# Kernel tuning notes

Measured on AMD Instinct MI355X. Metric: run time of the kernel, lower is better.

## Reference

```python
import jax, jax.numpy as jnp
import numpy as np

NEG_SLOPE = 0.01  # torch nn.LeakyReLU default


def setup_inputs() -> dict:
    key = jax.random.key(0)
    k1, k2, k3, k4, k5 = jax.random.split(key, 5)
    B, C, N, O = 32, 512, 1024, 512
    x = jax.random.normal(k1, (B, C, N), dtype=jnp.float32)
    wq = jax.random.normal(k2, (C,), dtype=jnp.float32) * (1.0 / np.sqrt(C))
    wk = jax.random.normal(k3, (C,), dtype=jnp.float32) * (1.0 / np.sqrt(C))
    wm = jax.random.normal(k4, (O, C), dtype=jnp.float32) * (1.0 / np.sqrt(C))
    bm = jax.random.normal(k5, (O,), dtype=jnp.float32) * 0.01
    return {"x": x, "wq": wq, "wk": wk, "wm": wm, "bm": bm}


def reference(x, wq, wk, wm, bm):
    # x: [B, C, N]
    q = jnp.einsum('c,bcn->bn', wq, x)            # [B, N] (Conv1d C->1, k=1, no bias)
    k = jnp.einsum('c,bcn->bn', wk, x)            # [B, N]
    scores = q[:, None, :] + k[:, :, None]        # [B, N, N] additive broadcast
    scores = jnp.where(scores > 0, scores, NEG_SLOPE * scores)  # LeakyReLU
    att = jax.nn.softmax(scores, axis=-1)         # softmax over last dim
    agg = jnp.einsum('bcn,bmn->bcm', x, att)      # weighted aggregation [B, C, N]
    out = jnp.einsum('oc,bcm->bom', wm, agg) + bm[None, :, None]  # Conv1d k=1
    return jax.nn.relu(out)
```

## Files before the change

### kernel.cpp

```cpp
#include <hip/hip_runtime.h>


constexpr int B = 32, C = 512, N = 1024, O = 512;
constexpr float L2E = 1.4426950408889634f;

typedef _Float16 half8 __attribute__((ext_vector_type(8)));
typedef _Float16 half4v __attribute__((ext_vector_type(4)));
typedef _Float16 half2v __attribute__((ext_vector_type(2)));
typedef float f32x4 __attribute__((ext_vector_type(4)));

#if __has_builtin(__builtin_amdgcn_exp2f)
#define EXP2(x) __builtin_amdgcn_exp2f(x)
#else
#define EXP2(x) exp2f(x)
#endif

__device__ __forceinline__ half8 cvt8(float4 a, float4 b) {
  half8 h;
  h[0] = (_Float16)a.x; h[1] = (_Float16)a.y; h[2] = (_Float16)a.z; h[3] = (_Float16)a.w;
  h[4] = (_Float16)b.x; h[5] = (_Float16)b.y; h[6] = (_Float16)b.z; h[7] = (_Float16)b.w;
  return h;
}

__device__ __forceinline__ unsigned fenc(float x) {
  unsigned u = __float_as_uint(x);
  return (u & 0x80000000u) ? ~u : (u ^ 0x80000000u);
}
__device__ __forceinline__ float fdec(unsigned e) {
  unsigned u = (e & 0x80000000u) ? (e ^ 0x80000000u) : ~e;
  return __uint_as_float(u);
}

__global__ __launch_bounds__(256) void wmh_kernel(const float* __restrict__ wm,
                                                  _Float16* __restrict__ wmh) {
  int i = (blockIdx.x * 256 + threadIdx.x) * 8;
  float4 a = *(const float4*)(wm + i);
  float4 b = *(const float4*)(wm + i + 4);
  *(half8*)(wmh + i) = cvt8(a, b);
}

__global__ __launch_bounds__(256) void gemm_y_kernel(const float* __restrict__ x,
    const _Float16* __restrict__ wmh, const float* __restrict__ wq,
    const float* __restrict__ wk, float* __restrict__ q, float* __restrict__ k,
    unsigned* __restrict__ qmax_u, _Float16* __restrict__ Yt) {
  __shared__ half2v Xs[16 * 130];
  __shared__ float mred[4];
  int b  = blockIdx.y;
  int n0 = blockIdx.x * 128;
  int o0 = blockIdx.z * 128;
  int t = threadIdx.x;
  int w = t >> 6, l = t & 63;
  int nw = w >> 1, ow = w & 1;
  int lm = l & 15, q8 = (l >> 4) * 8, q4 = (l >> 4) * 4;

  int cp = t >> 4, ng = t & 15;
  bool doqk = (blockIdx.z == 0);
  float aq[8] = {}, ak[8] = {};

  const _Float16* wb[4];
#pragma unroll
  for (int j = 0; j < 4; ++j)
    wb[j] = wmh + (size_t)(o0 + ow * 64 + j * 16 + lm) * C + q8;

  f32x4 acc[4][4] = {};
  for (int c0 = 0; c0 < C; c0 += 32) {
    const float* xr = x + ((size_t)b * C + c0 + 2 * cp) * N + n0 + ng * 8;
    float4 a0 = *(const float4*)(xr);
    float4 a1 = *(const float4*)(xr + 4);
    float4 b0 = *(const float4*)(xr + N);
    float4 b1 = *(const float4*)(xr + N + 4);
    half8 bf[4];
#pragma unroll
    for (int j = 0; j < 4; ++j) bf[j] = *(const half8*)(wb[j] + c0);

    if (doqk) {
      float2 wq2 = *(const float2*)&wq[c0 + 2 * cp];
      float2 wk2 = *(const float2*)&wk[c0 + 2 * cp];
      aq[0] = fmaf(wq2.x, a0.x, fmaf(wq2.y, b0.x, aq[0]));
      aq[1] = fmaf(wq2.x, a0.y, fmaf(wq2.y, b0.y, aq[1]));
      aq[2] = fmaf(wq2.x, a0.z, fmaf(wq2.y, b0.z, aq[2]));
      aq[3] = fmaf(wq2.x, a0.w, fmaf(wq2.y, b0.w, aq[3]));
      aq[4] = fmaf(wq2.x, a1.x, fmaf(wq2.y, b1.x, aq[4]));
      aq[5] = fmaf(wq2.x, a1.y, fmaf(wq2.y, b1.y, aq[5]));
      aq[6] = fmaf(wq2.x, a1.z, fmaf(wq2.y, b1.z, aq[6]));
      aq[7] = fmaf(wq2.x, a1.w, fmaf(wq2.y, b1.w, aq[7]));
      ak[0] = fmaf(wk2.x, a0.x, fmaf(wk2.y, b0.x, ak[0]));
      ak[1] = fmaf(wk2.x, a0.y, fmaf(wk2.y, b0.y, ak[1]));
      ak[2] = fmaf(wk2.x, a0.z, fmaf(wk2.y, b0.z, ak[2]));
      ak[3] = fmaf(wk2.x, a0.w, fmaf(wk2.y, b0.w, ak[3]));
      ak[4] = fmaf(wk2.x, a1.x, fmaf(wk2.y, b1.x, ak[4]));
      ak[5] = fmaf(wk2.x, a1.y, fmaf(wk2.y, b1.y, ak[5]));
      ak[6] = fmaf(wk2.x, a1.z, fmaf(wk2.y, b1.z, ak[6]));
      ak[7] = fmaf(wk2.x, a1.w, fmaf(wk2.y, b1.w, ak[7]));
    }

    __syncthreads();
    {
      half2v* xp = &Xs[cp * 130 + ng * 8];
      xp[0] = half2v{(_Float16)a0.x, (_Float16)b0.x};
      xp[1] = half2v{(_Float16)a0.y, (_Float16)b0.y};
      xp[2] = half2v{(_Float16)a0.z, (_Float16)b0.z};
      xp[3] = half2v{(_Float16)a0.w, (_Float16)b0.w};
      xp[4] = half2v{(_Float16)a1.x, (_Float16)b1.x};
      xp[5] = half2v{(_Float16)a1.y, (_Float16)b1.y};
      xp[6] = half2v{(_Float16)a1.z, (_Float16)b1.z};
      xp[7] = half2v{(_Float16)a1.w, (_Float16)b1.w};
    }
    __syncthreads();

    half8 af[4];
#pragma unroll
    for (int i = 0; i < 4; ++i) {
      int nrow = nw * 64 + i * 16 + lm;
#pragma unroll
      for (int jp = 0; jp < 4; ++jp) {
        half2v p = Xs[(q4 + jp) * 130 + nrow];
        af[i][2 * jp]     = p[0];
        af[i][2 * jp + 1] = p[1];
      }
    }
#pragma unroll
    for (int i = 0; i < 4; ++i)
#pragma unroll
      for (int j = 0; j < 4; ++j)
        acc[i][j] = __builtin_amdgcn_mfma_f32_16x16x32_f16(af[i], bf[j], acc[i][j], 0, 0, 0);
  }

#pragma unroll
  for (int i = 0; i < 4; ++i) {
    int n_b = n0 + nw * 64 + i * 16 + (l >> 4) * 4;
#pragma unroll
    for (int j = 0; j < 4; ++j) {
      int o_c = o0 + ow * 64 + j * 16 + lm;
      half4v h;
      h[0] = (_Float16)acc[i][j][0];
      h[1] = (_Float16)acc[i][j][1];
      h[2] = (_Float16)acc[i][j][2];
      h[3] = (_Float16)acc[i][j][3];
      *(half4v*)&Yt[((size_t)b * O + o_c) * N + n_b] = h;
    }
  }

  if (doqk) {
    float* red = (float*)Xs;
    float qv_final = -1e30f;
    __syncthreads();
#pragma unroll
    for (int j = 0; j < 8; ++j) red[cp * 130 + ng * 8 + j] = aq[j];
    __syncthreads();
    if (t < 128) {
      float s = 0.f;
#pragma unroll
      for (int p = 0; p < 16; ++p) s += red[p * 130 + t];
      qv_final = L2E * s;
      q[b * N + n0 + t] = qv_final;
    }
    __syncthreads();
#pragma unroll
    for (int j = 0; j < 8; ++j) red[cp * 130 + ng * 8 + j] = ak[j];
    __syncthreads();
    if (t < 128) {
      float s = 0.f;
#pragma unroll
      for (int p = 0; p < 16; ++p) s += red[p * 130 + t];
      k[b * N + n0 + t] = L2E * s;
    }
    float m = qv_final;
#pragma unroll
    for (int off = 32; off > 0; off >>= 1) m = fmaxf(m, __shfl_down(m, off, 64));
    if ((t & 63) == 0) mred[t >> 6] = m;
    __syncthreads();
    if (t == 0) {
      float bmax = fmaxf(fmaxf(mred[0], mred[1]), fmaxf(mred[2], mred[3]));
      atomicMax(&qmax_u[b], fenc(bmax));
    }
  }
}

__global__ __launch_bounds__(256) void gemm_out_kernel(const _Float16* __restrict__ Yt,
    const float* __restrict__ q, const float* __restrict__ k,
    const unsigned* __restrict__ qmax_u, const float* __restrict__ bm,
    float* __restrict__ out) {
  __shared__ __align__(16) float qs[N];
  __shared__ __align__(16) _Float16 Ys[128 * 40];
  __shared__ float izs[128];
  int b  = blockIdx.y;
  int o0 = blockIdx.x * 128;
  int m0 = blockIdx.z * 128;
  int t = threadIdx.x;
  int w = t >> 6, l = t & 63;
  int lm = l & 15, g = l >> 4, q8 = g * 8;

  *(float4*)&qs[t * 4] = *(const float4*)&q[b * N + t * 4];

  float qmv = fdec(qmax_u[b]);
  float k2[2], k3[2];
#pragma unroll
  for (int i = 0; i < 2; ++i) {
    float km = k[b * N + m0 + w * 32 + i * 16 + lm];
    float s0 = qmv + km;
    float M  = fmaxf(s0, 0.01f * s0);
    k2[i] = km - M;
    k3[i] = fmaf(0.01f, km, -M);
  }
  half8 ones;
#pragma unroll
  for (int jj = 0; jj < 8; ++jj) ones[jj] = (_Float16)1.0f;
  f32x4 acc_z[2] = {};
  int yr = t >> 1, yp = t & 1;
  const _Float16* ysrc = Yt + ((size_t)b * O + o0 + yr) * N + yp * 16;
  __syncthreads();

  f32x4 acc[2][8] = {};
  for (int n0k = 0; n0k < N; n0k += 32) {
    half8 y0 = *(const half8*)(ysrc + n0k);
    half8 y1 = *(const half8*)(ysrc + n0k + 8);
    float4 qa = *(const float4*)&qs[n0k + q8];
    float4 qb = *(const float4*)&qs[n0k + q8 + 4];
    float qv[8] = {qa.x, qa.y, qa.z, qa.w, qb.x, qb.y, qb.z, qb.w};
    half8 af[2];
#pragma unroll
    for (int i = 0; i < 2; ++i) {
#pragma unroll
      for (int jj = 0; jj < 8; ++jj) {
        float arg = fmaxf(qv[jj] + k2[i], fmaf(0.01f, qv[jj], k3[i]));
        af[i][jj] = (_Float16)EXP2(arg);
      }
      acc_z[i] = __builtin_amdgcn_mfma_f32_16x16x32_f16(af[i], ones, acc_z[i], 0, 0, 0);
    }
    __syncthreads();
    *(half8*)&Ys[yr * 40 + yp * 16]     = y0;
    *(half8*)&Ys[yr * 40 + yp * 16 + 8] = y1;
    __syncthreads();

    half8 bf[8];
#pragma unroll
    for (int j = 0; j < 8; ++j)
      bf[j] = *(const half8*)&Ys[(j * 16 + lm) * 40 + q8];
#pragma unroll
    for (int i = 0; i < 2; ++i)
#pragma unroll
      for (int j = 0; j < 8; ++j)
        acc[i][j] = __builtin_amdgcn_mfma_f32_16x16x32_f16(af[i], bf[j], acc[i][j], 0, 0, 0);
  }

  if (lm == 0) {
#pragma unroll
    for (int i = 0; i < 2; ++i) {
#pragma unroll
      for (int r = 0; r < 4; ++r)
        izs[w * 32 + i * 16 + g * 4 + r] = 1.0f / acc_z[i][r];
    }
  }
  __syncthreads();

  float iz4v[2][4];
#pragma unroll
  for (int i = 0; i < 2; ++i) {
    float4 iz4 = *(const float4*)&izs[w * 32 + i * 16 + g * 4];
    iz4v[i][0] = iz4.x; iz4v[i][1] = iz4.y; iz4v[i][2] = iz4.z; iz4v[i][3] = iz4.w;
  }
#pragma unroll
  for (int j = 0; j < 8; ++j) {
    int o_c = o0 + j * 16 + lm;
    float bias = bm[o_c];
#pragma unroll
    for (int i = 0; i < 2; ++i) {
      int m_b = m0 + w * 32 + i * 16 + g * 4;
      float4 r;
      r.x = fmaxf(fmaf(acc[i][j][0], iz4v[i][0], bias), 0.f);
      r.y = fmaxf(fmaf(acc[i][j][1], iz4v[i][1], bias), 0.f);
      r.z = fmaxf(fmaf(acc[i][j][2], iz4v[i][2], bias), 0.f);
      r.w = fmaxf(fmaf(acc[i][j][3], iz4v[i][3], bias), 0.f);
      *(float4*)&out[((size_t)b * O + o_c) * N + m_b] = r;
    }
  }
}

extern "C" void kernel_launch(void* const* d_in, const int* in_sizes, int n_in,
                              void* d_out, int out_size, void* d_ws, size_t ws_size,
                              hipStream_t stream) {
  const float* x  = (const float*)d_in[0];
  const float* wq = (const float*)d_in[1];
  const float* wk = (const float*)d_in[2];
  const float* wm = (const float*)d_in[3];
  const float* bm = (const float*)d_in[4];
  float* out = (float*)d_out;

  float* q    = (float*)d_ws;
  float* k    = q + B * N;
  unsigned* qmax_u = (unsigned*)(k + B * N);
  _Float16* wmh = (_Float16*)(qmax_u + 64);
  _Float16* Yt  = wmh + (size_t)O * C;

  hipMemsetAsync(qmax_u, 0, 64 * sizeof(unsigned), stream);
  wmh_kernel<<<dim3(O * C / (256 * 8)), 256, 0, stream>>>(wm, wmh);
  gemm_y_kernel<<<dim3(N / 128, B, O / 128), 256, 0, stream>>>(x, wmh, wq, wk, q, k, qmax_u, Yt);
  gemm_out_kernel<<<dim3(O / 128, B, N / 128), 256, 0, stream>>>(Yt, q, k, qmax_u, bm, out);
}
```

Measured before the change: 216.3 us.

## Widen output-GEMM tile to 256 o-columns with 512 threads, drop memset

The output GEMM kernel now covers 256 output channels per block with 8 waves, each wave owning 16 m-rows instead of 32. Each wave therefore computes the exp-softmax weights once and reuses them across 16 column tiles, which cuts the redundant exp work per output across o-blocks in half. The qmax reset memset is folded into the weight-conversion kernel, saving one launch. In exchange the block uses more LDS and more accumulator registers per thread, which may lower occupancy.

Result: faster. 210.4 us (-2.7%).

```diff
diff --git a/kernel.cpp b/kernel.cpp
--- a/kernel.cpp
+++ b/kernel.cpp
@@ -32,11 +32,13 @@
 }
 
 __global__ __launch_bounds__(256) void wmh_kernel(const float* __restrict__ wm,
-                                                  _Float16* __restrict__ wmh) {
+                                                  _Float16* __restrict__ wmh,
+                                                  unsigned* __restrict__ qmax_u) {
   int i = (blockIdx.x * 256 + threadIdx.x) * 8;
   float4 a = *(const float4*)(wm + i);
   float4 b = *(const float4*)(wm + i + 4);
   *(half8*)(wmh + i) = cvt8(a, b);
+  if (blockIdx.x == 0 && threadIdx.x < 64) qmax_u[threadIdx.x] = 0u;
 }
 
 __global__ __launch_bounds__(256) void gemm_y_kernel(const float* __restrict__ x,
@@ -177,103 +179,83 @@
   }
 }
 
-__global__ __launch_bounds__(256) void gemm_out_kernel(const _Float16* __restrict__ Yt,
+__global__ __launch_bounds__(512) void gemm_out_kernel(const _Float16* __restrict__ Yt,
     const float* __restrict__ q, const float* __restrict__ k,
     const unsigned* __restrict__ qmax_u, const float* __restrict__ bm,
     float* __restrict__ out) {
   __shared__ __align__(16) float qs[N];
-  __shared__ __align__(16) _Float16 Ys[128 * 40];
+  __shared__ __align__(16) _Float16 Ys[256 * 40];
   __shared__ float izs[128];
   int b  = blockIdx.y;
-  int o0 = blockIdx.x * 128;
+  int o0 = blockIdx.x * 256;
   int m0 = blockIdx.z * 128;
   int t = threadIdx.x;
   int w = t >> 6, l = t & 63;
   int lm = l & 15, g = l >> 4, q8 = g * 8;
 
-  *(float4*)&qs[t * 4] = *(const float4*)&q[b * N + t * 4];
+  *(float2*)&qs[t * 2] = *(const float2*)&q[b * N + t * 2];
 
   float qmv = fdec(qmax_u[b]);
-  float k2[2], k3[2];
-#pragma unroll
-  for (int i = 0; i < 2; ++i) {
-    float km = k[b * N + m0 + w * 32 + i * 16 + lm];
-    float s0 = qmv + km;
-    float M  = fmaxf(s0, 0.01f * s0);
-    k2[i] = km - M;
-    k3[i] = fmaf(0.01f, km, -M);
-  }
+  float km = k[b * N + m0 + w * 16 + lm];
+  float s0 = qmv + km;
+  float M  = fmaxf(s0, 0.01f * s0);
+  float k2 = km - M;
+  float k3 = fmaf(0.01f, km, -M);
+
   half8 ones;
 #pragma unroll
   for (int jj = 0; jj < 8; ++jj) ones[jj] = (_Float16)1.0f;
-  f32x4 acc_z[2] = {};
+  f32x4 acc_z = {};
   int yr = t >> 1, yp = t & 1;
   const _Float16* ysrc = Yt + ((size_t)b * O + o0 + yr) * N + yp * 16;
   __syncthreads();
 
-  f32x4 acc[2][8] = {};
+  f32x4 acc[16] = {};
   for (int n0k = 0; n0k < N; n0k += 32) {
     half8 y0 = *(const half8*)(ysrc + n0k);
     half8 y1 = *(const half8*)(ysrc + n0k + 8);
     float4 qa = *(const float4*)&qs[n0k + q8];
     float4 qb = *(const float4*)&qs[n0k + q8 + 4];
     float qv[8] = {qa.x, qa.y, qa.z, qa.w, qb.x, qb.y, qb.z, qb.w};
-    half8 af[2];
-#pragma unroll
-    for (int i = 0; i < 2; ++i) {
-#pragma unroll
-      for (int jj = 0; jj < 8; ++jj) {
-        float arg = fmaxf(qv[jj] + k2[i], fmaf(0.01f, qv[jj], k3[i]));
-        af[i][jj] = (_Float16)EXP2(arg);
-      }
-      acc_z[i] = __builtin_amdgcn_mfma_f32_16x16x32_f16(af[i], ones, acc_z[i], 0, 0, 0);
-    }
+    half8 af;
+#pragma unroll
+    for (int jj = 0; jj < 8; ++jj) {
+      float arg = fmaxf(qv[jj] + k2, fmaf(0.01f, qv[jj], k3));
+      af[jj] = (_Float16)EXP2(arg);
+    }
+    acc_z = __builtin_amdgcn_mfma_f32_16x16x32_f16(af, ones, acc_z, 0, 0, 0);
+
     __syncthreads();
     *(half8*)&Ys[yr * 40 + yp * 16]     = y0;
     *(half8*)&Ys[yr * 40 + yp * 16 + 8] = y1;
     __syncthreads();
 
-    half8 bf[8];
-#pragma unroll
-    for (int j = 0; j < 8; ++j)
-      bf[j] = *(const half8*)&Ys[(j * 16 + lm) * 40 + q8];
-#pragma unroll
-    for (int i = 0; i < 2; ++i)
-#pragma unroll
-      for (int j = 0; j < 8; ++j)
-        acc[i][j] = __builtin_amdgcn_mfma_f32_16x16x32_f16(af[i], bf[j], acc[i][j], 0, 0, 0);
+#pragma unroll
+    for (int j = 0; j < 16; ++j) {
+      half8 bf = *(const half8*)&Ys[(j * 16 + lm) * 40 + q8];
+      acc[j] = __builtin_amdgcn_mfma_f32_16x16x32_f16(af, bf, acc[j], 0, 0, 0);
+    }
   }
 
   if (lm == 0) {
 #pragma unroll
-    for (int i = 0; i < 2; ++i) {
-#pragma unroll
-      for (int r = 0; r < 4; ++r)
-        izs[w * 32 + i * 16 + g * 4 + r] = 1.0f / acc_z[i][r];
-    }
+    for (int r = 0; r < 4; ++r)
+      izs[w * 16 + g * 4 + r] = 1.0f / acc_z[r];
   }
   __syncthreads();
 
-  float iz4v[2][4];
-#pragma unroll
-  for (int i = 0; i < 2; ++i) {
-    float4 iz4 = *(const float4*)&izs[w * 32 + i * 16 + g * 4];
-    iz4v[i][0] = iz4.x; iz4v[i][1] = iz4.y; iz4v[i][2] = iz4.z; iz4v[i][3] = iz4.w;
-  }
-#pragma unroll
-  for (int j = 0; j < 8; ++j) {
+  float4 iz4 = *(const float4*)&izs[w * 16 + g * 4];
+#pragma unroll
+  for (int j = 0; j < 16; ++j) {
     int o_c = o0 + j * 16 + lm;
     float bias = bm[o_c];
-#pragma unroll
-    for (int i = 0; i < 2; ++i) {
-      int m_b = m0 + w * 32 + i * 16 + g * 4;
-      float4 r;
-      r.x = fmaxf(fmaf(acc[i][j][0], iz4v[i][0], bias), 0.f);
-      r.y = fmaxf(fmaf(acc[i][j][1], iz4v[i][1], bias), 0.f);
-      r.z = fmaxf(fmaf(acc[i][j][2], iz4v[i][2], bias), 0.f);
-      r.w = fmaxf(fmaf(acc[i][j][3], iz4v[i][3], bias), 0.f);
-      *(float4*)&out[((size_t)b * O + o_c) * N + m_b] = r;
-    }
+    int m_b = m0 + w * 16 + g * 4;
+    float4 r;
+    r.x = fmaxf(fmaf(acc[j][0], iz4.x, bias), 0.f);
+    r.y = fmaxf(fmaf(acc[j][1], iz4.y, bias), 0.f);
+    r.z = fmaxf(fmaf(acc[j][2], iz4.z, bias), 0.f);
+    r.w = fmaxf(fmaf(acc[j][3], iz4.w, bias), 0.f);
+    *(float4*)&out[((size_t)b * O + o_c) * N + m_b] = r;
   }
 }
 
@@ -293,8 +275,7 @@
   _Float16* wmh = (_Float16*)(qmax_u + 64);
   _Float16* Yt  = wmh + (size_t)O * C;
 
-  hipMemsetAsync(qmax_u, 0, 64 * sizeof(unsigned), stream);
-  wmh_kernel<<<dim3(O * C / (256 * 8)), 256, 0, stream>>>(wm, wmh);
+  wmh_kernel<<<dim3(O * C / (256 * 8)), 256, 0, stream>>>(wm, wmh, qmax_u);
   gemm_y_kernel<<<dim3(N / 128, B, O / 128), 256, 0, stream>>>(x, wmh, wq, wk, q, k, qmax_u, Yt);
-  gemm_out_kernel<<<dim3(O / 128, B, N / 128), 256, 0, stream>>>(Yt, q, k, qmax_u, bm, out);
-}
+  gemm_out_kernel<<<dim3(O / 256, B, N / 128), 512, 0, stream>>>(Yt, q, k, qmax_u, bm, out);
+}
```
